# Kernel tuning notes

Hardware: AMD Instinct MI355X
Metric: run time of the kernel (lower is better)

The kernel has to match this reference:

```python
import jax, jax.numpy as jnp
import numpy as np

DIM = 1024
NUM_HEADS = 16
HEAD_DIM = DIM // NUM_HEADS
MAX_LEN = 2048
ROPE_BASE = 10000.0


def _rope_tables(n, d, base=ROPE_BASE):
    inv_freq = 1.0 / (base ** (np.arange(0, d, 2, dtype=np.float32) / d))  # [d/2]
    t = np.arange(n, dtype=np.float32)
    freqs = np.outer(t, inv_freq)  # [n, d/2]
    return jnp.asarray(np.cos(freqs)), jnp.asarray(np.sin(freqs))


def _apply_rotary(x, cos, sin):
    # x: [B, H, N, D]; pairs are consecutive elements (2i, 2i+1)
    xe = x[..., 0::2]
    xo = x[..., 1::2]
    # cos/sin: [N, D/2] -> broadcast over B, H
    oe = xe * cos - xo * sin
    oo = xe * sin + xo * cos
    return jnp.stack([oe, oo], axis=-1).reshape(x.shape)


def setup_inputs() -> dict:
    key = jax.random.key(0)
    ks = jax.random.split(key, 11)
    B, T, S = 4, 2048, 2048
    sc = 1.0 / np.sqrt(DIM)
    inp = {
        "query": jax.random.normal(ks[0], (B, T, DIM), jnp.float32),
        "key": jax.random.normal(ks[1], (B, S, DIM), jnp.float32),
        "value": jax.random.normal(ks[2], (B, S, DIM), jnp.float32),
        "Wq": jax.random.normal(ks[3], (DIM, DIM), jnp.float32) * sc,
        "bq": jnp.zeros((DIM,), jnp.float32),
        "Wk": jax.random.normal(ks[4], (DIM, DIM), jnp.float32) * sc,
        "bk": jnp.zeros((DIM,), jnp.float32),
        "Wv": jax.random.normal(ks[5], (DIM, DIM), jnp.float32) * sc,
        "bv": jnp.zeros((DIM,), jnp.float32),
        "Wo": jax.random.normal(ks[6], (DIM, DIM), jnp.float32) * sc,
        "bo": jnp.zeros((DIM,), jnp.float32),
    }
    return inp


def reference(query, key, value, Wq, bq, Wk, bk, Wv, bv, Wo, bo):
    B, T, C = query.shape
    S = key.shape[1]
    H, D = NUM_HEADS, HEAD_DIM
    scale = D ** -0.5

    q = (query @ Wq + bq).reshape(B, T, H, D).transpose(0, 2, 1, 3)  # [B,H,T,D]
    k = (key @ Wk + bk).reshape(B, S, H, D).transpose(0, 2, 1, 3)    # [B,H,S,D]
    v = (value @ Wv + bv).reshape(B, S, H, D).transpose(0, 2, 1, 3)  # [B,H,S,D]

    cos, sin = _rope_tables(max(T, S), D)
    q = _apply_rotary(q, cos[:T], sin[:T])
    k = _apply_rotary(k, cos[:S], sin[:S])

    scores = jnp.einsum("bhtd,bhsd->bhts", q, k) * scale  # [B,H,T,S]
    causal = jnp.tril(jnp.ones((T, S), bool))
    scores = jnp.where(causal[None, None], scores, -jnp.inf)
    att = jax.nn.softmax(scores, axis=-1)

    out = jnp.einsum("bhts,bhsd->bhtd", att, v)  # [B,H,T,D]
    out = out.transpose(0, 2, 1, 3).reshape(B, T, C)
    return out @ Wo + bo
```

## Files before the change

kernel.cpp:

```cpp
#include <hip/hip_runtime.h>
#include <cstdint>
#include <math.h>

typedef __bf16 bf16_t;
typedef __bf16 bf16x8 __attribute__((ext_vector_type(8)));
typedef __bf16 bf16x4 __attribute__((ext_vector_type(4)));
typedef float f32x4 __attribute__((ext_vector_type(4)));

#define MFMA16(a, b, c) __builtin_amdgcn_mfma_f32_16x16x32_bf16((a), (b), (c), 0, 0, 0)

static constexpr int BATCH = 4;
static constexpr int SEQ = 2048;
static constexpr int DIMC = 1024;
static constexpr int NH = 16;
static constexpr int HD = 64;

__device__ __forceinline__ void async_copy16(void* lds, const void* g) {
    __builtin_amdgcn_global_load_lds(
        (const __attribute__((address_space(1))) void*)g,
        (__attribute__((address_space(3))) void*)lds, 16, 0, 0);
}

__device__ __forceinline__ float fast_exp2(float x) {
#if __has_builtin(__builtin_amdgcn_exp2f)
    return __builtin_amdgcn_exp2f(x);
#else
    return __expf(x * 0.6931471805599453f);
#endif
}

__global__ __launch_bounds__(256) void cvt3(const float* __restrict__ q,
                                            const float* __restrict__ k,
                                            const float* __restrict__ v,
                                            bf16_t* __restrict__ out) {
    const float* in = (blockIdx.y == 0) ? q : ((blockIdx.y == 1) ? k : v);
    bf16_t* o = out + (size_t)blockIdx.y * BATCH * SEQ * DIMC;
    const int i = blockIdx.x * 256 + threadIdx.x;
    const float4 f0 = ((const float4*)in)[i * 2];
    const float4 f1 = ((const float4*)in)[i * 2 + 1];
    bf16x8 vv;
    vv[0] = (bf16_t)f0.x; vv[1] = (bf16_t)f0.y; vv[2] = (bf16_t)f0.z; vv[3] = (bf16_t)f0.w;
    vv[4] = (bf16_t)f1.x; vv[5] = (bf16_t)f1.y; vv[6] = (bf16_t)f1.z; vv[7] = (bf16_t)f1.w;
    ((bf16x8*)o)[i] = vv;
}

__global__ __launch_bounds__(256) void transpose_cvt(const float* __restrict__ W0,
                                                     const float* __restrict__ W1,
                                                     const float* __restrict__ W2,
                                                     const float* __restrict__ W3,
                                                     bf16_t* __restrict__ out) {
    const float* Ws[4] = {W0, W1, W2, W3};
    const float* W = Ws[blockIdx.z];
    bf16_t* Wt = out + (size_t)blockIdx.z * DIMC * DIMC;
    __shared__ float tile[32][33];
    const int tx = threadIdx.x & 31;
    const int ty = threadIdx.x >> 5;
    const int x0 = blockIdx.x * 32;
    const int y0 = blockIdx.y * 32;
    #pragma unroll
    for (int j = ty; j < 32; j += 8)
        tile[j][tx] = W[(size_t)(y0 + j) * DIMC + x0 + tx];
    __syncthreads();
    #pragma unroll
    for (int j = ty; j < 32; j += 8)
        Wt[(size_t)(x0 + j) * DIMC + y0 + tx] = (bf16_t)tile[tx][j];
}

__global__ __launch_bounds__(256) void rope_tab(float* __restrict__ cosT, float* __restrict__ sinT) {
    const int idx = blockIdx.x * 256 + threadIdx.x;
    const int t = idx >> 5;
    const int p = idx & 31;
    const float inv = exp2f(-0.41524101186092029f * (float)p);
    const float ang = (float)t * inv;
    float s, c;
    sincosf(ang, &s, &c);
    cosT[idx] = c;
    sinT[idx] = s;
}

#define GEMM_KLOOP(A_, Bt_)                                                             \
    f32x4 acc[4][4] = {};                                                               \
    const int swW = ((lane >> 2) & 3) ^ ((lane >> 4) & 3);         \
    const int rIn = lane >> 2;                                    \
    const int gW = ((lane & 3) ^ swW) * 8;                        \
    const int fR = (l15 & 3) ^ ((l15 >> 2) & 3);                    \
    for (int kt = 0; kt < DIMC / 32; ++kt) {                                            \
        const int k0 = kt * 32;                                                         \
        __syncthreads();                                                                \
        _Pragma("unroll") for (int ci = 0; ci < 2; ++ci) {                              \
            const int c = 2 * w + ci;                                                   \
            async_copy16(&Bs[c * 512], Bt_ + (size_t)(col0 + c * 16 + rIn) * DIMC + k0 + gW); \
            async_copy16(&As[c * 512], A_ + (size_t)(row0 + c * 16 + rIn) * DIMC + k0 + gW);  \
        }                                                                               \
        __syncthreads();                                                                \
        bf16x8 af[4], bfr[4];                                                           \
        _Pragma("unroll") for (int mt = 0; mt < 4; ++mt)                                \
            af[mt] = *(const bf16x8*)&As[(wr * 64 + mt * 16 + l15) * 32 + ((quad ^ fR) << 3)]; \
        _Pragma("unroll") for (int nt = 0; nt < 4; ++nt)                                \
            bfr[nt] = *(const bf16x8*)&Bs[(wc * 64 + nt * 16 + l15) * 32 + ((quad ^ fR) << 3)]; \
        _Pragma("unroll") for (int mt = 0; mt < 4; ++mt)                                \
            _Pragma("unroll") for (int nt = 0; nt < 4; ++nt)                            \
                acc[mt][nt] = MFMA16(af[mt], bfr[nt], acc[mt][nt]);                     \
    }

__global__ __launch_bounds__(256) void gemm_qkv(const bf16_t* __restrict__ Cb,
                                                const bf16_t* __restrict__ Wt3,
                                                const float* __restrict__ bq,
                                                const float* __restrict__ bk,
                                                const float* __restrict__ bv,
                                                bf16_t* __restrict__ Qr,
                                                bf16_t* __restrict__ Kr,
                                                bf16_t* __restrict__ Vr,
                                                const float* __restrict__ cosT,
                                                const float* __restrict__ sinT) {
    __shared__ bf16_t As[128 * 32];
    __shared__ bf16_t Bs[128 * 32];
    const int z = blockIdx.z;
    const bf16_t* A = Cb + (size_t)z * BATCH * SEQ * DIMC;
    const bf16_t* Bt = Wt3 + (size_t)z * DIMC * DIMC;
    const float* bias = (z == 0) ? bq : ((z == 1) ? bk : bv);
    bf16_t* outp = (z == 0) ? Qr : ((z == 1) ? Kr : Vr);
    const bool rope = (z < 2);
    const int tid = threadIdx.x;
    const int w = tid >> 6;
    const int lane = tid & 63;
    const int l15 = lane & 15;
    const int quad = lane >> 4;
    const int wr = w >> 1, wc = w & 1;
    const int row0 = blockIdx.y * 128, col0 = blockIdx.x * 128;
    GEMM_KLOOP(A, Bt)
    #pragma unroll
    for (int nt = 0; nt < 4; ++nt) {
        const int col = col0 + wc * 64 + nt * 16 + l15;
        const float bvl = bias[col];
        const int h = col >> 6;
        const int d = col & 63;
        #pragma unroll
        for (int mt = 0; mt < 4; ++mt) {
            #pragma unroll
            for (int r = 0; r < 4; ++r) {
                const int row = row0 + wr * 64 + mt * 16 + quad * 4 + r;
                const int t = row & (SEQ - 1);
                const int bb = row >> 11;
                float v = acc[mt][nt][r] + bvl;
                float o = v;
                if (rope) {
                    const int p = d >> 1;
                    const float cs = cosT[t * 32 + p];
                    const float sn = sinT[t * 32 + p];
                    const float partner = __shfl_xor(v, 1);
                    o = (d & 1) ? (partner * sn + v * cs) : (v * cs - partner * sn);
                }
                outp[(((size_t)bb * NH + h) * SEQ + t) * HD + d] = (bf16_t)o;
            }
        }
    }
}

__global__ __launch_bounds__(256) void gemm_o(const bf16_t* __restrict__ A,
                                              const bf16_t* __restrict__ Bt,
                                              const float* __restrict__ bias,
                                              float* __restrict__ out) {
    __shared__ bf16_t As[128 * 32];
    __shared__ bf16_t Bs[128 * 32];
    const int tid = threadIdx.x;
    const int w = tid >> 6;
    const int lane = tid & 63;
    const int l15 = lane & 15;
    const int quad = lane >> 4;
    const int wr = w >> 1, wc = w & 1;
    const int row0 = blockIdx.y * 128, col0 = blockIdx.x * 128;
    GEMM_KLOOP(A, Bt)
    #pragma unroll
    for (int nt = 0; nt < 4; ++nt) {
        const int col = col0 + wc * 64 + nt * 16 + l15;
        const float bvl = bias[col];
        #pragma unroll
        for (int mt = 0; mt < 4; ++mt) {
            #pragma unroll
            for (int r = 0; r < 4; ++r) {
                const int row = row0 + wr * 64 + mt * 16 + quad * 4 + r;
                out[(size_t)row * DIMC + col] = acc[mt][nt][r] + bvl;
            }
        }
    }
}

__global__ __launch_bounds__(256) void attn_kernel(const bf16_t* __restrict__ Qr,
                                                   const bf16_t* __restrict__ Kr,
                                                   const bf16_t* __restrict__ Vr,
                                                   bf16_t* __restrict__ O) {
    __shared__ bf16_t Ks[64 * 64];
    __shared__ bf16_t Vt[64 * 72];
    __shared__ bf16_t Ps[4][32 * 72];
    const int tid = threadIdx.x;
    const int w = tid >> 6;
    const int lane = tid & 63;
    const int l15 = lane & 15;
    const int quad = lane >> 4;
    const int bh = blockIdx.y;
    const int b = bh >> 4, h = bh & 15;
    const bf16_t* Qb = Qr + (size_t)bh * SEQ * HD;
    const bf16_t* Kb = Kr + (size_t)bh * SEQ * HD;
    const bf16_t* Vb = Vr + (size_t)bh * SEQ * HD;
    const float S2 = 0.18033688011112043f;

    bf16x8 ones;
    #pragma unroll
    for (int j8 = 0; j8 < 8; ++j8) ones[j8] = (bf16_t)1.0f;
    bf16x8 idB[2];
    #pragma unroll
    for (int ch = 0; ch < 2; ++ch)
        #pragma unroll
        for (int j8 = 0; j8 < 8; ++j8)
            idB[ch][j8] = (quad * 8 + j8 == ch * 16 + l15) ? (bf16_t)1.0f : (bf16_t)0.0f;

    const int sIn = lane >> 3;
    const int gK = ((lane & 7) ^ sIn) * 8;
    const int fK = (l15 & 7);

    for (int half = 0; half < 2; ++half) {
        const int j = (half == 0) ? blockIdx.x : 15 - blockIdx.x;
        const int q0 = j * 128;
        bf16x8 qa[2][2];
        #pragma unroll
        for (int mg = 0; mg < 2; ++mg)
            #pragma unroll
            for (int kc = 0; kc < 2; ++kc)
                qa[mg][kc] = *(const bf16x8*)(Qb + (size_t)(q0 + mg * 64 + w * 16 + l15) * HD +
                                              kc * 32 + quad * 8);
        f32x4 acco[2][4] = {};
        f32x4 accl[2] = {};
        const int nIter = 2 * j + 2;
        for (int it = 0; it < nIter; ++it) {
            const int s0 = it * 64;
            __syncthreads();
            #pragma unroll
            for (int ci = 0; ci < 2; ++ci) {
                const int c = 2 * w + ci;
                async_copy16(&Ks[c * 512], Kb + (size_t)(s0 + c * 8 + sIn) * HD + gK);
            }
            {
                const bf16_t* vsrc = Vb + (size_t)(s0 + w * 16 + l15) * HD + quad * 8;
                bf16x8 av0 = *(const bf16x8*)(vsrc);
                bf16x8 av1 = *(const bf16x8*)(vsrc + 32);
                #pragma unroll
                for (int c = 0; c < 4; ++c) {
                    f32x4 zz = {};
                    f32x4 tv = MFMA16((c < 2) ? av0 : av1, idB[c & 1], zz);
                    bf16x4 pk;
                    #pragma unroll
                    for (int r = 0; r < 4; ++r) pk[r] = (bf16_t)tv[r];
                    *(bf16x4*)&Vt[(c * 16 + l15) * 72 + w * 16 + quad * 4] = pk;
                }
            }
            __syncthreads();
            bf16x8 kb[4][2];
            #pragma unroll
            for (int mt = 0; mt < 4; ++mt)
                #pragma unroll
                for (int kc = 0; kc < 2; ++kc)
                    kb[mt][kc] = *(const bf16x8*)&Ks[(mt * 16 + l15) * 64 +
                                                     (((kc * 4 + quad) ^ fK) << 3)];
            #pragma unroll
            for (int mg = 0; mg < 2; ++mg) {
                if (mg == 0 && it == 2 * j + 1) continue;
                const bool diag = (it == 2 * j + mg);
                #pragma unroll
                for (int mt = 0; mt < 4; ++mt) {
                    f32x4 z = {};
                    z = MFMA16(kb[mt][0], qa[mg][0], z);
                    z = MFMA16(kb[mt][1], qa[mg][1], z);
                    bf16x4 pk;
                    #pragma unroll
                    for (int r = 0; r < 4; ++r) {
                        float v = z[r];
                        if (diag && (mt * 16 + quad * 4 + r > w * 16 + l15)) v = -INFINITY;
                        pk[r] = (bf16_t)fast_exp2(S2 * v);
                    }
                    *(bf16x4*)&Ps[w][(mg * 16 + l15) * 72 + mt * 16 + quad * 4] = pk;
                }
            }
            asm volatile("s_waitcnt lgkmcnt(0)" ::: "memory");
            bf16x8 vb[4][2];
            #pragma unroll
            for (int dt = 0; dt < 4; ++dt)
                #pragma unroll
                for (int kc = 0; kc < 2; ++kc)
                    vb[dt][kc] = *(const bf16x8*)&Vt[(dt * 16 + l15) * 72 + kc * 32 + quad * 8];
            #pragma unroll
            for (int mg = 0; mg < 2; ++mg) {
                if (mg == 0 && it == 2 * j + 1) continue;
                const bf16x8 pa0 = *(const bf16x8*)&Ps[w][(mg * 16 + l15) * 72 + quad * 8];
                const bf16x8 pa1 = *(const bf16x8*)&Ps[w][(mg * 16 + l15) * 72 + 32 + quad * 8];
                #pragma unroll
                for (int dt = 0; dt < 4; ++dt) {
                    acco[mg][dt] = MFMA16(pa0, vb[dt][0], acco[mg][dt]);
                    acco[mg][dt] = MFMA16(pa1, vb[dt][1], acco[mg][dt]);
                }
                accl[mg] = MFMA16(pa0, ones, accl[mg]);
                accl[mg] = MFMA16(pa1, ones, accl[mg]);
            }
        }
        #pragma unroll
        for (int mg = 0; mg < 2; ++mg) {
            #pragma unroll
            for (int r = 0; r < 4; ++r) {
                const float inv = 1.0f / accl[mg][r];
                const int trow = q0 + mg * 64 + w * 16 + quad * 4 + r;
                bf16_t* orow = O + ((size_t)(b * SEQ + trow)) * DIMC + h * HD;
                #pragma unroll
                for (int dt = 0; dt < 4; ++dt)
                    orow[dt * 16 + l15] = (bf16_t)(acco[mg][dt][r] * inv);
            }
        }
    }
}

extern "C" void kernel_launch(void* const* d_in, const int* in_sizes, int n_in,
                              void* d_out, int out_size, void* d_ws, size_t ws_size,
                              hipStream_t stream) {
    const float* query = (const float*)d_in[0];
    const float* key = (const float*)d_in[1];
    const float* value = (const float*)d_in[2];
    const float* Wq = (const float*)d_in[3];
    const float* bq = (const float*)d_in[4];
    const float* Wk = (const float*)d_in[5];
    const float* bk = (const float*)d_in[6];
    const float* Wv = (const float*)d_in[7];
    const float* bv = (const float*)d_in[8];
    const float* Wo = (const float*)d_in[9];
    const float* bo = (const float*)d_in[10];

    char* ws = (char*)d_ws;
    const size_t WT_BYTES = (size_t)DIMC * DIMC * sizeof(bf16_t);
    const size_t ACT_BYTES = (size_t)BATCH * SEQ * DIMC * sizeof(bf16_t);
    bf16_t* WT = (bf16_t*)ws;
    bf16_t* WoT = WT + 3 * (size_t)DIMC * DIMC;
    float* cosT = (float*)(ws + 4 * WT_BYTES);
    float* sinT = (float*)(ws + 4 * WT_BYTES + 262144);
    bf16_t* Cb = (bf16_t*)(ws + 4 * WT_BYTES + 2 * 262144);
    bf16_t* Qr = (bf16_t*)((char*)Cb + 3 * ACT_BYTES);
    bf16_t* Kr = (bf16_t*)((char*)Cb + 4 * ACT_BYTES);
    bf16_t* Vr = (bf16_t*)((char*)Cb + 5 * ACT_BYTES);
    bf16_t* Ob = Cb;

    transpose_cvt<<<dim3(32, 32, 4), 256, 0, stream>>>(Wq, Wk, Wv, Wo, WT);
    rope_tab<<<dim3(256), 256, 0, stream>>>(cosT, sinT);
    cvt3<<<dim3(4096, 3), 256, 0, stream>>>(query, key, value, Cb);
    gemm_qkv<<<dim3(DIMC / 128, (BATCH * SEQ) / 128, 3), 256, 0, stream>>>(
        Cb, WT, bq, bk, bv, Qr, Kr, Vr, cosT, sinT);
    attn_kernel<<<dim3(8, BATCH * NH), 256, 0, stream>>>(Qr, Kr, Vr, Ob);
    gemm_o<<<dim3(DIMC / 128, (BATCH * SEQ) / 128), 256, 0, stream>>>(Ob, WoT, bo, (float*)d_out);
}
```

Baseline: 372.6 us.

## Stage QKV epilogue through LDS for vectorized stores and remap block order

The QKV GEMM epilogue now writes accumulators plus bias into shared memory, and each thread then reads 16 contiguous columns of one row. It applies RoPE with vectorized cos/sin loads and writes two 16-byte bf16 chunks, replacing scattered 2-byte stores and per-element shuffles. Both GEMMs remap block indices so consecutive blocks walk down rows for a fixed column tile, and attention swaps grid axes so heads are adjacent. These changes target uncoalesced global stores and aim for better L2 reuse, at the cost of extra LDS round trips and barriers in the epilogue.

```diff
diff --git a/kernel.cpp b/kernel.cpp
--- a/kernel.cpp
+++ b/kernel.cpp
@@ -113,8 +113,10 @@
                                                 bf16_t* __restrict__ Vr,
                                                 const float* __restrict__ cosT,
                                                 const float* __restrict__ sinT) {
-    __shared__ bf16_t As[128 * 32];
-    __shared__ bf16_t Bs[128 * 32];
+    __shared__ __align__(16) unsigned char smem[32 * 132 * 4];
+    bf16_t* As = (bf16_t*)smem;
+    bf16_t* Bs = (bf16_t*)(smem + 8192);
+    float* eps = (float*)smem;
     const int z = blockIdx.z;
     const bf16_t* A = Cb + (size_t)z * BATCH * SEQ * DIMC;
     const bf16_t* Bt = Wt3 + (size_t)z * DIMC * DIMC;
@@ -127,33 +129,63 @@
     const int l15 = lane & 15;
     const int quad = lane >> 4;
     const int wr = w >> 1, wc = w & 1;
-    const int row0 = blockIdx.y * 128, col0 = blockIdx.x * 128;
+    const int raw = blockIdx.y * 8 + blockIdx.x;
+    const int row0 = (raw & 63) * 128, col0 = (raw >> 6) * 128;
     GEMM_KLOOP(A, Bt)
-    #pragma unroll
-    for (int nt = 0; nt < 4; ++nt) {
-        const int col = col0 + wc * 64 + nt * 16 + l15;
-        const float bvl = bias[col];
-        const int h = col >> 6;
-        const int d = col & 63;
-        #pragma unroll
-        for (int mt = 0; mt < 4; ++mt) {
-            #pragma unroll
-            for (int r = 0; r < 4; ++r) {
-                const int row = row0 + wr * 64 + mt * 16 + quad * 4 + r;
-                const int t = row & (SEQ - 1);
-                const int bb = row >> 11;
-                float v = acc[mt][nt][r] + bvl;
-                float o = v;
-                if (rope) {
-                    const int p = d >> 1;
-                    const float cs = cosT[t * 32 + p];
-                    const float sn = sinT[t * 32 + p];
-                    const float partner = __shfl_xor(v, 1);
-                    o = (d & 1) ? (partner * sn + v * cs) : (v * cs - partner * sn);
-                }
-                outp[(((size_t)bb * NH + h) * SEQ + t) * HD + d] = (bf16_t)o;
-            }
-        }
+    float bvl[4];
+    #pragma unroll
+    for (int nt = 0; nt < 4; ++nt) bvl[nt] = bias[col0 + wc * 64 + nt * 16 + l15];
+    const int lr = tid >> 3;
+    const int cg = tid & 7;
+    const int c0 = cg * 16;
+    const int h = (col0 + c0) >> 6;
+    const int dbase = (col0 + c0) & 63;
+    #pragma unroll
+    for (int p = 0; p < 4; ++p) {
+        __syncthreads();
+        #pragma unroll
+        for (int nt = 0; nt < 4; ++nt)
+            #pragma unroll
+            for (int r = 0; r < 4; ++r)
+                eps[(wr * 16 + quad * 4 + r) * 132 + wc * 64 + nt * 16 + l15] =
+                    acc[p][nt][r] + bvl[nt];
+        __syncthreads();
+        const int grow = row0 + (lr >> 4) * 64 + p * 16 + (lr & 15);
+        const int t = grow & (SEQ - 1);
+        const int bb = grow >> 11;
+        float vals[16];
+        #pragma unroll
+        for (int q4 = 0; q4 < 4; ++q4) {
+            f32x4 vv = *(const f32x4*)&eps[lr * 132 + c0 + q4 * 4];
+            vals[q4 * 4 + 0] = vv[0]; vals[q4 * 4 + 1] = vv[1];
+            vals[q4 * 4 + 2] = vv[2]; vals[q4 * 4 + 3] = vv[3];
+        }
+        bf16x8 o0, o1;
+        if (rope) {
+            const int pbase = t * 32 + (dbase >> 1);
+            const float4 cs0 = *(const float4*)&cosT[pbase];
+            const float4 cs1 = *(const float4*)&cosT[pbase + 4];
+            const float4 sn0 = *(const float4*)&sinT[pbase];
+            const float4 sn1 = *(const float4*)&sinT[pbase + 4];
+            const float cc[8] = {cs0.x, cs0.y, cs0.z, cs0.w, cs1.x, cs1.y, cs1.z, cs1.w};
+            const float ss[8] = {sn0.x, sn0.y, sn0.z, sn0.w, sn1.x, sn1.y, sn1.z, sn1.w};
+            #pragma unroll
+            for (int i = 0; i < 8; ++i) {
+                const float e = vals[2 * i], o = vals[2 * i + 1];
+                const float oe = e * cc[i] - o * ss[i];
+                const float oo = e * ss[i] + o * cc[i];
+                if (i < 4) { o0[2 * i] = (bf16_t)oe; o0[2 * i + 1] = (bf16_t)oo; }
+                else { o1[2 * (i - 4)] = (bf16_t)oe; o1[2 * (i - 4) + 1] = (bf16_t)oo; }
+            }
+        } else {
+            #pragma unroll
+            for (int i = 0; i < 8; ++i) o0[i] = (bf16_t)vals[i];
+            #pragma unroll
+            for (int i = 0; i < 8; ++i) o1[i] = (bf16_t)vals[8 + i];
+        }
+        bf16_t* dst = outp + (((size_t)bb * NH + h) * SEQ + t) * HD + dbase;
+        *(bf16x8*)dst = o0;
+        *(bf16x8*)(dst + 8) = o1;
     }
 }
 
@@ -161,15 +193,17 @@
                                               const bf16_t* __restrict__ Bt,
                                               const float* __restrict__ bias,
                                               float* __restrict__ out) {
-    __shared__ bf16_t As[128 * 32];
-    __shared__ bf16_t Bs[128 * 32];
+    __shared__ __align__(16) unsigned char smem[16384];
+    bf16_t* As = (bf16_t*)smem;
+    bf16_t* Bs = (bf16_t*)(smem + 8192);
     const int tid = threadIdx.x;
     const int w = tid >> 6;
     const int lane = tid & 63;
     const int l15 = lane & 15;
     const int quad = lane >> 4;
     const int wr = w >> 1, wc = w & 1;
-    const int row0 = blockIdx.y * 128, col0 = blockIdx.x * 128;
+    const int raw = blockIdx.y * 8 + blockIdx.x;
+    const int row0 = (raw & 63) * 128, col0 = (raw >> 6) * 128;
     GEMM_KLOOP(A, Bt)
     #pragma unroll
     for (int nt = 0; nt < 4; ++nt) {
@@ -198,7 +232,7 @@
     const int lane = tid & 63;
     const int l15 = lane & 15;
     const int quad = lane >> 4;
-    const int bh = blockIdx.y;
+    const int bh = blockIdx.x;
     const int b = bh >> 4, h = bh & 15;
     const bf16_t* Qb = Qr + (size_t)bh * SEQ * HD;
     const bf16_t* Kb = Kr + (size_t)bh * SEQ * HD;
@@ -220,7 +254,7 @@
     const int fK = (l15 & 7);
 
     for (int half = 0; half < 2; ++half) {
-        const int j = (half == 0) ? blockIdx.x : 15 - blockIdx.x;
+        const int j = (half == 0) ? blockIdx.y : 15 - blockIdx.y;
         const int q0 = j * 128;
         bf16x8 qa[2][2];
         #pragma unroll
@@ -350,6 +384,6 @@
     cvt3<<<dim3(4096, 3), 256, 0, stream>>>(query, key, value, Cb);
     gemm_qkv<<<dim3(DIMC / 128, (BATCH * SEQ) / 128, 3), 256, 0, stream>>>(
         Cb, WT, bq, bk, bv, Qr, Kr, Vr, cosT, sinT);
-    attn_kernel<<<dim3(8, BATCH * NH), 256, 0, stream>>>(Qr, Kr, Vr, Ob);
+    attn_kernel<<<dim3(BATCH * NH, 8), 256, 0, stream>>>(Qr, Kr, Vr, Ob);
     gemm_o<<<dim3(DIMC / 128, (BATCH * SEQ) / 128), 256, 0, stream>>>(Ob, WoT, bo, (float*)d_out);
 }
```

Result: faster. 340.1 us (-8.7%).
